# Kernel optimization log

Hardware: AMD Instinct MI355X
Metric: run time of the kernel (lower is better)

## Reference

```python
import jax, jax.numpy as jnp
import numpy as np

N_NODES = 50000
N_EDGES = 800000
IN_DIM = 128
HID_DIM = 128
N_GRAPHS = 512


def setup_inputs() -> dict:
    key = jax.random.key(0)
    ks = jax.random.split(key, 8)
    x = jax.random.normal(ks[0], (N_NODES, IN_DIM), dtype=jnp.float32)
    edge_index = jax.random.randint(ks[1], (2, N_EDGES), 0, N_NODES, dtype=jnp.int64)
    batch = jnp.sort(jax.random.randint(ks[2], (N_NODES,), 0, N_GRAPHS, dtype=jnp.int64))
    x_source = jax.random.randint(ks[3], (N_NODES,), 0, 2, dtype=jnp.int64)
    s1 = 1.0 / np.sqrt(IN_DIM)
    s2 = 1.0 / np.sqrt(HID_DIM)
    W1 = jax.random.normal(ks[4], (IN_DIM, HID_DIM), dtype=jnp.float32) * s1
    b1 = jnp.zeros((HID_DIM,), dtype=jnp.float32)
    W2 = jax.random.normal(ks[5], (HID_DIM, HID_DIM), dtype=jnp.float32) * s2
    b2 = jnp.zeros((HID_DIM,), dtype=jnp.float32)
    Wh = jax.random.normal(ks[6], (HID_DIM + IN_DIM, 2), dtype=jnp.float32) * (1.0 / np.sqrt(HID_DIM + IN_DIM))
    bh = jnp.zeros((2,), dtype=jnp.float32)
    return {"x": x, "edge_index": edge_index, "batch": batch, "x_source": x_source,
            "W1": W1, "b1": b1, "W2": W2, "b2": b2, "Wh": Wh, "bh": bh}


def _gcn_conv(x, W, b, src, dst, deg_inv_sqrt):
    # PyG GCNConv: h = x W; out[i] = sum_{j->i} norm_ij h[j] + norm_ii h[i] + b
    # with self-loops and symmetric normalization norm_ij = d_i^{-1/2} d_j^{-1/2}
    h = x @ W                                        # [N, out]
    norm_e = deg_inv_sqrt[src] * deg_inv_sqrt[dst]    # [E]
    msg = h[src] * norm_e[:, None]                    # gather + scale
    agg = jax.ops.segment_sum(msg, dst, num_segments=x.shape[0])
    agg = agg + h * (deg_inv_sqrt ** 2)[:, None]      # self-loop term
    return agg + b


def _mean_pool(x, seg, num_segments):
    sums = jax.ops.segment_sum(x, seg, num_segments=num_segments)
    cnt = jax.ops.segment_sum(jnp.ones((x.shape[0],), x.dtype), seg, num_segments=num_segments)
    return sums / jnp.maximum(cnt, 1.0)[:, None]


def reference(x, edge_index, batch, x_source, W1, b1, W2, b2, Wh, bh):
    src, dst = edge_index[0], edge_index[1]
    # degree with self-loops (edge weights = 1)
    deg = jax.ops.segment_sum(jnp.ones((src.shape[0],), x.dtype), dst,
                              num_segments=x.shape[0]) + 1.0
    deg_inv_sqrt = jax.lax.rsqrt(deg)

    h = jax.nn.relu(_gcn_conv(x, W1, b1, src, dst, deg_inv_sqrt))
    # dropout is identity in eval mode
    h = jax.nn.relu(_gcn_conv(h, W2, b2, src, dst, deg_inv_sqrt))

    gnn_emb = _mean_pool(h, batch, N_GRAPHS)          # [G, hid]

    # CodeBERT pooling: masked mean of raw node features where x_source == 1
    mask = (x_source == 1).astype(x.dtype)            # [N]
    summed = jax.ops.segment_sum(x * mask[:, None], batch, num_segments=N_GRAPHS)
    counts = jnp.maximum(jax.ops.segment_sum(mask, batch, num_segments=N_GRAPHS), 1.0)
    codebert_emb = summed / counts[:, None]           # [G, in]

    emb = jnp.concatenate([gnn_emb, codebert_emb], axis=1)  # [G, hid+in]
    return emb @ Wh + bh                              # [G, 2]
```

## Files before the change

### kernel.cpp

```cpp
#include <hip/hip_runtime.h>
#include <hip/hip_fp16.h>

#define NNODES 50000
#define NEDGES 800000
#define DIM    128
#define NGRAPH 512
#define NB_SCAN 196
#define NSLAB  3125

typedef _Float16 f16x8 __attribute__((ext_vector_type(8)));
typedef float    f32x4 __attribute__((ext_vector_type(4)));
union U4H8 { uint4 u; f16x8 h; };

__global__ void prep(int4* __restrict__ degp4,
                     const float* __restrict__ W1, const float* __restrict__ W2,
                     __half* __restrict__ Wt1, __half* __restrict__ Wt2) {
    int t = blockIdx.x * 256 + threadIdx.x;
    if (t < NNODES * 4) { degp4[t] = make_int4(0, 0, 0, 0); return; }
    int i = t - NNODES * 4;
    if (i >= 4096) return;
    const float* W = (i < 2048) ? W1 : W2;
    __half* Wt = (i < 2048) ? Wt1 : Wt2;
    int j = i & 2047;
    int c  = j >> 4;
    int k0 = (j & 15) * 8;
    __half tmp[8];
    #pragma unroll
    for (int u = 0; u < 8; ++u) tmp[u] = (__half)W[(size_t)(k0 + u) * DIM + c];
    *(uint4*)(Wt + (size_t)c * DIM + k0) = *(uint4*)tmp;
}

__global__ void edge_pos(const int4* __restrict__ dst4, int* __restrict__ degp,
                         int4* __restrict__ pos4, int n4) {
    int t = blockIdx.x * blockDim.x + threadIdx.x;
    if (t >= n4) return;
    int4 d = dst4[t];
    int4 p;
    p.x = atomicAdd(&degp[d.x << 4], 1);
    p.y = atomicAdd(&degp[d.y << 4], 1);
    p.z = atomicAdd(&degp[d.z << 4], 1);
    p.w = atomicAdd(&degp[d.w << 4], 1);
    pos4[t] = p;
}

__global__ void scan_block(const int* __restrict__ degp, int* __restrict__ out,
                           int* __restrict__ partials, float* __restrict__ dis, int n) {
    __shared__ int s[256];
    int t = threadIdx.x;
    int gid = blockIdx.x * 256 + t;
    int v = (gid < n) ? degp[gid << 4] : 0;
    if (gid < n) dis[gid] = rsqrtf((float)v + 1.0f);
    s[t] = v;
    __syncthreads();
    #pragma unroll
    for (int off = 1; off < 256; off <<= 1) {
        int u = (t >= off) ? s[t - off] : 0;
        __syncthreads();
        s[t] += u;
        __syncthreads();
    }
    if (gid < n) out[gid] = s[t] - v;
    if (t == 255) partials[blockIdx.x] = s[255];
}

__global__ void scan_partials(const int* __restrict__ in, int* __restrict__ out, int n) {
    __shared__ int s[256];
    int t = threadIdx.x;
    int v = (t < n) ? in[t] : 0;
    s[t] = v;
    __syncthreads();
    #pragma unroll
    for (int off = 1; off < 256; off <<= 1) {
        int u = (t >= off) ? s[t - off] : 0;
        __syncthreads();
        s[t] += u;
        __syncthreads();
    }
    if (t < n) out[t] = s[t] - v;
}

__global__ void edge_scatter2(const int4* __restrict__ src4, const int4* __restrict__ dst4,
                              const int4* __restrict__ pos4, const int* __restrict__ rowstart,
                              const int* __restrict__ part2, int* __restrict__ csr_src, int n4) {
    int t = blockIdx.x * blockDim.x + threadIdx.x;
    if (t >= n4) return;
    int4 s = src4[t];
    int4 d = dst4[t];
    int4 p = pos4[t];
    csr_src[rowstart[d.x] + part2[d.x >> 8] + p.x] = s.x;
    csr_src[rowstart[d.y] + part2[d.y >> 8] + p.y] = s.y;
    csr_src[rowstart[d.z] + part2[d.z >> 8] + p.z] = s.z;
    csr_src[rowstart[d.w] + part2[d.w >> 8] + p.w] = s.w;
}

template<typename XT>
__global__ void __launch_bounds__(256) gemm_mfma(const XT* __restrict__ X,
                                                 const __half* __restrict__ Wt,
                                                 const float* __restrict__ dis,
                                                 __half* __restrict__ Y) {
    __shared__ __align__(16) unsigned char Wl[128 * 256];

    const int t = threadIdx.x;
    {
        int col = t >> 1;
        int kb0 = (t & 1) * 128;
        const unsigned char* g = (const unsigned char*)Wt + col * 256 + kb0;
        #pragma unroll
        for (int i = 0; i < 8; ++i) {
            uint4 v = *(const uint4*)(g + i * 16);
            int kb = kb0 + i * 16;
            *(uint4*)(Wl + col * 256 + (kb ^ ((col & 7) << 4))) = v;
        }
    }
    __syncthreads();

    int wave = t >> 6;
    int slab = blockIdx.x * 4 + wave;
    if (slab >= NSLAB) return;
    int l  = t & 63;
    int lr = l & 15;
    int lg = l >> 4;

    int arow = slab * 16 + lr;

    f16x8 afr[4];
    if constexpr (sizeof(XT) == 4) {
        const float* xr = (const float*)X + (size_t)arow * DIM;
        #pragma unroll
        for (int c = 0; c < 4; ++c) {
            int k0 = c * 32 + lg * 8;
            float4 u0 = *(const float4*)(xr + k0);
            float4 u1 = *(const float4*)(xr + k0 + 4);
            f16x8 a;
            a[0] = (_Float16)u0.x; a[1] = (_Float16)u0.y;
            a[2] = (_Float16)u0.z; a[3] = (_Float16)u0.w;
            a[4] = (_Float16)u1.x; a[5] = (_Float16)u1.y;
            a[6] = (_Float16)u1.z; a[7] = (_Float16)u1.w;
            afr[c] = a;
        }
    } else {
        const __half* xr = (const __half*)X + (size_t)arow * DIM;
        #pragma unroll
        for (int c = 0; c < 4; ++c) {
            U4H8 u; u.u = *(const uint4*)(xr + c * 32 + lg * 8);
            afr[c] = u.h;
        }
    }

    f32x4 acc[8];
    #pragma unroll
    for (int jt = 0; jt < 8; ++jt) acc[jt] = (f32x4){0.f, 0.f, 0.f, 0.f};

    #pragma unroll
    for (int c = 0; c < 4; ++c) {
        #pragma unroll
        for (int jt = 0; jt < 8; ++jt) {
            int col = jt * 16 + lr;
            int kb  = c * 64 + lg * 16;
            U4H8 b;
            b.u = *(const uint4*)(Wl + col * 256 + (kb ^ ((col & 7) << 4)));
            acc[jt] = __builtin_amdgcn_mfma_f32_16x16x32_f16(afr[c], b.h, acc[jt], 0, 0, 0);
        }
    }

    float4 dv = *(const float4*)(dis + slab * 16 + lg * 4);
    float dsc[4] = {dv.x, dv.y, dv.z, dv.w};
    #pragma unroll
    for (int j = 0; j < 4; ++j) {
        int row = slab * 16 + lg * 4 + j;
        __half* yr = Y + (size_t)row * DIM + lr;
        #pragma unroll
        for (int jt = 0; jt < 8; ++jt)
            yr[jt * 16] = (__half)(acc[jt][j] * dsc[j]);
    }
}

__device__ __forceinline__ void acc_add(float4& a, uint2 u) {
    float2 f0 = __half22float2(*(__half2*)&u.x);
    float2 f1 = __half22float2(*(__half2*)&u.y);
    a.x += f0.x; a.y += f0.y; a.z += f1.x; a.w += f1.y;
}

__global__ void __launch_bounds__(256) gcn_gather(const __half* __restrict__ hwh,
                                                  const int* __restrict__ rowstart,
                                                  const int* __restrict__ part2,
                                                  const int* __restrict__ csr_src,
                                                  const float* __restrict__ dis,
                                                  const float* __restrict__ b,
                                                  __half* __restrict__ outh) {
    int t = blockIdx.x * 256 + threadIdx.x;
    int d = t >> 5, q = t & 31;
    if (d >= NNODES) return;
    const uint2* hw8 = (const uint2*)hwh;

    float4 a0 = make_float4(0.f, 0.f, 0.f, 0.f);
    float4 a1 = a0, a2 = a0, a3 = a0, a4 = a0, a5 = a0, a6 = a0, a7 = a0;

    acc_add(a0, hw8[(size_t)d * 32 + q]);

    int beg = rowstart[d] + part2[d >> 8];
    int end = (d + 1 < NNODES) ? rowstart[d + 1] + part2[(d + 1) >> 8] : NEDGES;
    int i = beg;
    for (; i + 8 <= end; i += 8) {
        int s0 = csr_src[i + 0], s1 = csr_src[i + 1];
        int s2 = csr_src[i + 2], s3 = csr_src[i + 3];
        int s4 = csr_src[i + 4], s5 = csr_src[i + 5];
        int s6 = csr_src[i + 6], s7 = csr_src[i + 7];
        uint2 v0 = hw8[(size_t)s0 * 32 + q];
        uint2 v1 = hw8[(size_t)s1 * 32 + q];
        uint2 v2 = hw8[(size_t)s2 * 32 + q];
        uint2 v3 = hw8[(size_t)s3 * 32 + q];
        uint2 v4 = hw8[(size_t)s4 * 32 + q];
        uint2 v5 = hw8[(size_t)s5 * 32 + q];
        uint2 v6 = hw8[(size_t)s6 * 32 + q];
        uint2 v7 = hw8[(size_t)s7 * 32 + q];
        acc_add(a0, v0); acc_add(a1, v1); acc_add(a2, v2); acc_add(a3, v3);
        acc_add(a4, v4); acc_add(a5, v5); acc_add(a6, v6); acc_add(a7, v7);
    }
    for (; i + 2 <= end; i += 2) {
        uint2 v0 = hw8[(size_t)csr_src[i + 0] * 32 + q];
        uint2 v1 = hw8[(size_t)csr_src[i + 1] * 32 + q];
        acc_add(a0, v0); acc_add(a1, v1);
    }
    if (i < end) acc_add(a0, hw8[(size_t)csr_src[i] * 32 + q]);

    a0.x += a1.x + a2.x + a3.x + a4.x + a5.x + a6.x + a7.x;
    a0.y += a1.y + a2.y + a3.y + a4.y + a5.y + a6.y + a7.y;
    a0.z += a1.z + a2.z + a3.z + a4.z + a5.z + a6.z + a7.z;
    a0.w += a1.w + a2.w + a3.w + a4.w + a5.w + a6.w + a7.w;

    float dd = dis[d];
    float4 bb = ((const float4*)b)[q];
    __half ot[4];
    ot[0] = (__half)fmaxf(fmaf(a0.x, dd, bb.x), 0.f);
    ot[1] = (__half)fmaxf(fmaf(a0.y, dd, bb.y), 0.f);
    ot[2] = (__half)fmaxf(fmaf(a0.z, dd, bb.z), 0.f);
    ot[3] = (__half)fmaxf(fmaf(a0.w, dd, bb.w), 0.f);
    ((uint2*)outh)[(size_t)d * 32 + q] = *(uint2*)ot;
}

__device__ __forceinline__ int lower_bound_i(const int* __restrict__ a, int n, int v) {
    int lo = 0, hi = n;
    while (lo < hi) {
        int mid = (lo + hi) >> 1;
        if (a[mid] < v) lo = mid + 1; else hi = mid;
    }
    return lo;
}

__global__ void __launch_bounds__(256) pool_head(const __half* __restrict__ h,
                                                 const float* __restrict__ x,
                                                 const int* __restrict__ batch,
                                                 const int* __restrict__ xsrc,
                                                 const float* __restrict__ Wh,
                                                 const float* __restrict__ bh,
                                                 float* __restrict__ out) {
    __shared__ float sAG[DIM];
    __shared__ float sAC[DIM];
    __shared__ int   sSC;
    int g   = blockIdx.x;
    int t   = threadIdx.x;
    int sub = t >> 5;
    int q   = t & 31;

    if (t < DIM) { sAG[t] = 0.f; sAC[t] = 0.f; }
    if (t == 0) sSC = 0;
    __syncthreads();

    int lo = lower_bound_i(batch, NNODES, g);
    int hi = lower_bound_i(batch, NNODES, g + 1);

    float4 ag = make_float4(0.f, 0.f, 0.f, 0.f);
    float4 ac = make_float4(0.f, 0.f, 0.f, 0.f);
    int sc = 0;
    const uint2* h8 = (const uint2*)h;
    const float4* x4 = (const float4*)x;
    for (int r = lo + sub; r < hi; r += 8) {
        acc_add(ag, h8[(size_t)r * 32 + q]);
        if (xsrc[r] == 1) {
            float4 xv = x4[(size_t)r * 32 + q];
            ac.x += xv.x; ac.y += xv.y; ac.z += xv.z; ac.w += xv.w;
            sc++;
        }
    }
    float* agp = sAG + q * 4;
    atomicAdd(agp + 0, ag.x); atomicAdd(agp + 1, ag.y);
    atomicAdd(agp + 2, ag.z); atomicAdd(agp + 3, ag.w);
    float* acp = sAC + q * 4;
    atomicAdd(acp + 0, ac.x); atomicAdd(acp + 1, ac.y);
    atomicAdd(acp + 2, ac.z); atomicAdd(acp + 3, ac.w);
    if (q == 0 && sc) atomicAdd(&sSC, sc);
    __syncthreads();

    if (t < 32) {
        float invg = 1.0f / fmaxf((float)(hi - lo), 1.0f);
        float invc = 1.0f / fmaxf((float)sSC, 1.0f);
        const float2* Wh2 = (const float2*)Wh;
        float a0 = 0.f, a1 = 0.f;
        #pragma unroll
        for (int j = 0; j < 4; ++j) {
            float e1 = sAG[t * 4 + j] * invg;
            float2 w1 = Wh2[t * 4 + j];
            a0 = fmaf(e1, w1.x, a0);
            a1 = fmaf(e1, w1.y, a1);
            float e2 = sAC[t * 4 + j] * invc;
            float2 w2 = Wh2[DIM + t * 4 + j];
            a0 = fmaf(e2, w2.x, a0);
            a1 = fmaf(e2, w2.y, a1);
        }
        #pragma unroll
        for (int off = 16; off; off >>= 1) {
            a0 += __shfl_down(a0, off, 32);
            a1 += __shfl_down(a1, off, 32);
        }
        if (t == 0) {
            out[g * 2 + 0] = a0 + bh[0];
            out[g * 2 + 1] = a1 + bh[1];
        }
    }
}

extern "C" void kernel_launch(void* const* d_in, const int* in_sizes, int n_in,
                              void* d_out, int out_size, void* d_ws, size_t ws_size,
                              hipStream_t stream) {
    const float* x     = (const float*)d_in[0];
    const int*   ei    = (const int*)d_in[1];
    const int*   batch = (const int*)d_in[2];
    const int*   xsrc  = (const int*)d_in[3];
    const float* W1 = (const float*)d_in[4];
    const float* b1 = (const float*)d_in[5];
    const float* W2 = (const float*)d_in[6];
    const float* b2 = (const float*)d_in[7];
    const float* Wh = (const float*)d_in[8];
    const float* bh = (const float*)d_in[9];
    float* out = (float*)d_out;

    const int* src = ei;
    const int* dst = ei + NEDGES;

    float* ws = (float*)d_ws;
    size_t off = 0;
    float*  dis      = ws + off;            off += 50048;
    int*    rowstart = (int*)(ws + off);    off += 50048;
    int*    degp     = (int*)(ws + off);    off += NNODES * 16;
    int*    part1    = (int*)(ws + off);    off += 256;
    int*    part2    = (int*)(ws + off);    off += 256;
    int*    pos      = (int*)(ws + off);    off += 800000;
    int*    csr_src  = (int*)(ws + off);    off += 800000;
    __half* Wt1      = (__half*)(ws + off); off += 8192;
    __half* Wt2      = (__half*)(ws + off); off += 8192;
    __half* hwh      = (__half*)(ws + off); off += (size_t)NNODES * DIM / 2;
    __half* hbuf     = (__half*)(ws + off); off += (size_t)NNODES * DIM / 2;

    const int n4 = NEDGES / 4;

    prep<<<(NNODES * 4 + 4096 + 255) / 256, 256, 0, stream>>>((int4*)degp, W1, W2, Wt1, Wt2);
    edge_pos<<<(n4 + 255) / 256, 256, 0, stream>>>((const int4*)dst, degp, (int4*)pos, n4);
    scan_block<<<NB_SCAN, 256, 0, stream>>>(degp, rowstart, part1, dis, NNODES);
    scan_partials<<<1, 256, 0, stream>>>(part1, part2, NB_SCAN);
    edge_scatter2<<<(n4 + 255) / 256, 256, 0, stream>>>((const int4*)src, (const int4*)dst,
                                                        (const int4*)pos, rowstart, part2,
                                                        csr_src, n4);

    const int ngemm = (NSLAB + 3) / 4;

    gemm_mfma<float><<<ngemm, 256, 0, stream>>>(x, Wt1, dis, hwh);
    gcn_gather<<<(NNODES * 32) / 256, 256, 0, stream>>>(hwh, rowstart, part2, csr_src, dis, b1, hbuf);

    gemm_mfma<__half><<<ngemm, 256, 0, stream>>>(hbuf, Wt2, dis, hwh);
    gcn_gather<<<(NNODES * 32) / 256, 256, 0, stream>>>(hwh, rowstart, part2, csr_src, dis, b2, hbuf);

    pool_head<<<NGRAPH, 256, 0, stream>>>(hbuf, x, batch, xsrc, Wh, bh, out);
}
```

Before: 173.6 us.

## Privatize degree counters into eight per-block-group copies to cut atomic contention

Result: slower. 177.9 us (+2.5%).

```diff
diff --git a/kernel.cpp b/kernel.cpp
--- a/kernel.cpp
+++ b/kernel.cpp
@@ -7,17 +7,20 @@
 #define NGRAPH 512
 #define NB_SCAN 196
 #define NSLAB  3125
+#define NPART  8
+#define CSTRIDE 50048
 
 typedef _Float16 f16x8 __attribute__((ext_vector_type(8)));
 typedef float    f32x4 __attribute__((ext_vector_type(4)));
 union U4H8 { uint4 u; f16x8 h; };
 
-__global__ void prep(int4* __restrict__ degp4,
+__global__ void prep(int4* __restrict__ cnt4,
                      const float* __restrict__ W1, const float* __restrict__ W2,
                      __half* __restrict__ Wt1, __half* __restrict__ Wt2) {
     int t = blockIdx.x * 256 + threadIdx.x;
-    if (t < NNODES * 4) { degp4[t] = make_int4(0, 0, 0, 0); return; }
-    int i = t - NNODES * 4;
+    const int nzero = NPART * CSTRIDE / 4;
+    if (t < nzero) { cnt4[t] = make_int4(0, 0, 0, 0); return; }
+    int i = t - nzero;
     if (i >= 4096) return;
     const float* W = (i < 2048) ? W1 : W2;
     __half* Wt = (i < 2048) ? Wt1 : Wt2;
@@ -30,26 +33,40 @@
     *(uint4*)(Wt + (size_t)c * DIM + k0) = *(uint4*)tmp;
 }
 
-__global__ void edge_pos(const int4* __restrict__ dst4, int* __restrict__ degp,
+__global__ void edge_pos(const int4* __restrict__ dst4, int* __restrict__ cnt8,
                          int4* __restrict__ pos4, int n4) {
     int t = blockIdx.x * blockDim.x + threadIdx.x;
     if (t >= n4) return;
+    int* c = cnt8 + (blockIdx.x & (NPART - 1)) * CSTRIDE;
     int4 d = dst4[t];
     int4 p;
-    p.x = atomicAdd(&degp[d.x << 4], 1);
-    p.y = atomicAdd(&degp[d.y << 4], 1);
-    p.z = atomicAdd(&degp[d.z << 4], 1);
-    p.w = atomicAdd(&degp[d.w << 4], 1);
+    p.x = atomicAdd(&c[d.x], 1);
+    p.y = atomicAdd(&c[d.y], 1);
+    p.z = atomicAdd(&c[d.z], 1);
+    p.w = atomicAdd(&c[d.w], 1);
     pos4[t] = p;
 }
 
-__global__ void scan_block(const int* __restrict__ degp, int* __restrict__ out,
-                           int* __restrict__ partials, float* __restrict__ dis, int n) {
+__global__ void scan_block(const int* __restrict__ cnt8, int* __restrict__ out,
+                           int* __restrict__ partials, float* __restrict__ dis,
+                           int* __restrict__ pre8, int n) {
     __shared__ int s[256];
     int t = threadIdx.x;
     int gid = blockIdx.x * 256 + t;
-    int v = (gid < n) ? degp[gid << 4] : 0;
-    if (gid < n) dis[gid] = rsqrtf((float)v + 1.0f);
+    int v = 0;
+    if (gid < n) {
+        int c[NPART];
+        #pragma unroll
+        for (int p = 0; p < NPART; ++p) c[p] = cnt8[p * CSTRIDE + gid];
+        int pr[NPART];
+        int run = 0;
+        #pragma unroll
+        for (int p = 0; p < NPART; ++p) { pr[p] = run; run += c[p]; }
+        v = run;
+        *(int4*)(pre8 + (size_t)gid * 8)     = make_int4(pr[0], pr[1], pr[2], pr[3]);
+        *(int4*)(pre8 + (size_t)gid * 8 + 4) = make_int4(pr[4], pr[5], pr[6], pr[7]);
+        dis[gid] = rsqrtf((float)v + 1.0f);
+    }
     s[t] = v;
     __syncthreads();
     #pragma unroll
@@ -81,16 +98,18 @@
 
 __global__ void edge_scatter2(const int4* __restrict__ src4, const int4* __restrict__ dst4,
                               const int4* __restrict__ pos4, const int* __restrict__ rowstart,
-                              const int* __restrict__ part2, int* __restrict__ csr_src, int n4) {
+                              const int* __restrict__ part2, const int* __restrict__ pre8,
+                              int* __restrict__ csr_src, int n4) {
     int t = blockIdx.x * blockDim.x + threadIdx.x;
     if (t >= n4) return;
+    int p = blockIdx.x & (NPART - 1);
     int4 s = src4[t];
     int4 d = dst4[t];
-    int4 p = pos4[t];
-    csr_src[rowstart[d.x] + part2[d.x >> 8] + p.x] = s.x;
-    csr_src[rowstart[d.y] + part2[d.y >> 8] + p.y] = s.y;
-    csr_src[rowstart[d.z] + part2[d.z >> 8] + p.z] = s.z;
-    csr_src[rowstart[d.w] + part2[d.w >> 8] + p.w] = s.w;
+    int4 q = pos4[t];
+    csr_src[rowstart[d.x] + part2[d.x >> 8] + pre8[(size_t)d.x * 8 + p] + q.x] = s.x;
+    csr_src[rowstart[d.y] + part2[d.y >> 8] + pre8[(size_t)d.y * 8 + p] + q.y] = s.y;
+    csr_src[rowstart[d.z] + part2[d.z >> 8] + pre8[(size_t)d.z * 8 + p] + q.z] = s.z;
+    csr_src[rowstart[d.w] + part2[d.w >> 8] + pre8[(size_t)d.w * 8 + p] + q.w] = s.w;
 }
 
 template<typename XT>
@@ -342,7 +361,8 @@
     size_t off = 0;
     float*  dis      = ws + off;            off += 50048;
     int*    rowstart = (int*)(ws + off);    off += 50048;
-    int*    degp     = (int*)(ws + off);    off += NNODES * 16;
+    int*    cnt8     = (int*)(ws + off);    off += NPART * CSTRIDE;
+    int*    pre8     = (int*)(ws + off);    off += 400384;
     int*    part1    = (int*)(ws + off);    off += 256;
     int*    part2    = (int*)(ws + off);    off += 256;
     int*    pos      = (int*)(ws + off);    off += 800000;
@@ -354,12 +374,12 @@
 
     const int n4 = NEDGES / 4;
 
-    prep<<<(NNODES * 4 + 4096 + 255) / 256, 256, 0, stream>>>((int4*)degp, W1, W2, Wt1, Wt2);
-    edge_pos<<<(n4 + 255) / 256, 256, 0, stream>>>((const int4*)dst, degp, (int4*)pos, n4);
-    scan_block<<<NB_SCAN, 256, 0, stream>>>(degp, rowstart, part1, dis, NNODES);
+    prep<<<(NPART * CSTRIDE / 4 + 4096 + 255) / 256, 256, 0, stream>>>((int4*)cnt8, W1, W2, Wt1, Wt2);
+    edge_pos<<<(n4 + 255) / 256, 256, 0, stream>>>((const int4*)dst, cnt8, (int4*)pos, n4);
+    scan_block<<<NB_SCAN, 256, 0, stream>>>(cnt8, rowstart, part1, dis, pre8, NNODES);
     scan_partials<<<1, 256, 0, stream>>>(part1, part2, NB_SCAN);
     edge_scatter2<<<(n4 + 255) / 256, 256, 0, stream>>>((const int4*)src, (const int4*)dst,
-                                                        (const int4*)pos, rowstart, part2,
+                                                        (const int4*)pos, rowstart, part2, pre8,
                                                         csr_src, n4);
 
     const int ngemm = (NSLAB + 3) / 4;
```

## Build CSR via two-level bucket sort instead of global atomic counting

Applied to the files above, without the earlier changes.

After: 151.1 us. 13.0% less time.

```diff
diff --git a/kernel.cpp b/kernel.cpp
--- a/kernel.cpp
+++ b/kernel.cpp
@@ -5,19 +5,21 @@
 #define NEDGES 800000
 #define DIM    128
 #define NGRAPH 512
-#define NB_SCAN 196
 #define NSLAB  3125
+#define EPB    1024
+#define NBLK_E 782
+#define NBUCK  196
+#define HSTRIDE NBLK_E
+#define NHIST  (NBUCK * HSTRIDE)
+#define NSB1   ((NHIST + 255) / 256)
 
 typedef _Float16 f16x8 __attribute__((ext_vector_type(8)));
 typedef float    f32x4 __attribute__((ext_vector_type(4)));
 union U4H8 { uint4 u; f16x8 h; };
 
-__global__ void prep(int4* __restrict__ degp4,
-                     const float* __restrict__ W1, const float* __restrict__ W2,
-                     __half* __restrict__ Wt1, __half* __restrict__ Wt2) {
-    int t = blockIdx.x * 256 + threadIdx.x;
-    if (t < NNODES * 4) { degp4[t] = make_int4(0, 0, 0, 0); return; }
-    int i = t - NNODES * 4;
+__global__ void prep_w(const float* __restrict__ W1, const float* __restrict__ W2,
+                       __half* __restrict__ Wt1, __half* __restrict__ Wt2) {
+    int i = blockIdx.x * 256 + threadIdx.x;
     if (i >= 4096) return;
     const float* W = (i < 2048) ? W1 : W2;
     __half* Wt = (i < 2048) ? Wt1 : Wt2;
@@ -30,67 +32,123 @@
     *(uint4*)(Wt + (size_t)c * DIM + k0) = *(uint4*)tmp;
 }
 
-__global__ void edge_pos(const int4* __restrict__ dst4, int* __restrict__ degp,
-                         int4* __restrict__ pos4, int n4) {
-    int t = blockIdx.x * blockDim.x + threadIdx.x;
-    if (t >= n4) return;
-    int4 d = dst4[t];
-    int4 p;
-    p.x = atomicAdd(&degp[d.x << 4], 1);
-    p.y = atomicAdd(&degp[d.y << 4], 1);
-    p.z = atomicAdd(&degp[d.z << 4], 1);
-    p.w = atomicAdd(&degp[d.w << 4], 1);
-    pos4[t] = p;
-}
-
-__global__ void scan_block(const int* __restrict__ degp, int* __restrict__ out,
-                           int* __restrict__ partials, float* __restrict__ dis, int n) {
+__global__ void __launch_bounds__(256) bucket_hist(const int* __restrict__ dst,
+                                                   int* __restrict__ hist) {
+    __shared__ int cnt[NBUCK];
+    int t = threadIdx.x;
+    if (t < NBUCK) cnt[t] = 0;
+    __syncthreads();
+    int e0 = blockIdx.x * EPB + t * 4;
+    if (e0 + 3 < NEDGES) {
+        int4 d = *(const int4*)(dst + e0);
+        atomicAdd(&cnt[d.x >> 8], 1);
+        atomicAdd(&cnt[d.y >> 8], 1);
+        atomicAdd(&cnt[d.z >> 8], 1);
+        atomicAdd(&cnt[d.w >> 8], 1);
+    }
+    __syncthreads();
+    if (t < NBUCK) hist[t * HSTRIDE + blockIdx.x] = cnt[t];
+}
+
+__global__ void sb1(const int* __restrict__ in, int* __restrict__ out,
+                    int* __restrict__ partials) {
     __shared__ int s[256];
     int t = threadIdx.x;
     int gid = blockIdx.x * 256 + t;
-    int v = (gid < n) ? degp[gid << 4] : 0;
-    if (gid < n) dis[gid] = rsqrtf((float)v + 1.0f);
+    int v = (gid < NHIST) ? in[gid] : 0;
     s[t] = v;
     __syncthreads();
     #pragma unroll
-    for (int off = 1; off < 256; off <<= 1) {
-        int u = (t >= off) ? s[t - off] : 0;
+    for (int o = 1; o < 256; o <<= 1) {
+        int u = (t >= o) ? s[t - o] : 0;
         __syncthreads();
         s[t] += u;
         __syncthreads();
     }
-    if (gid < n) out[gid] = s[t] - v;
+    if (gid < NHIST) out[gid] = s[t] - v;
     if (t == 255) partials[blockIdx.x] = s[255];
 }
 
-__global__ void scan_partials(const int* __restrict__ in, int* __restrict__ out, int n) {
-    __shared__ int s[256];
+__global__ void sb2(int* __restrict__ partials) {
+    __shared__ int s[1024];
     int t = threadIdx.x;
-    int v = (t < n) ? in[t] : 0;
+    int v = (t < NSB1) ? partials[t] : 0;
     s[t] = v;
     __syncthreads();
     #pragma unroll
-    for (int off = 1; off < 256; off <<= 1) {
-        int u = (t >= off) ? s[t - off] : 0;
+    for (int o = 1; o < 1024; o <<= 1) {
+        int u = (t >= o) ? s[t - o] : 0;
         __syncthreads();
         s[t] += u;
         __syncthreads();
     }
-    if (t < n) out[t] = s[t] - v;
-}
-
-__global__ void edge_scatter2(const int4* __restrict__ src4, const int4* __restrict__ dst4,
-                              const int4* __restrict__ pos4, const int* __restrict__ rowstart,
-                              const int* __restrict__ part2, int* __restrict__ csr_src, int n4) {
-    int t = blockIdx.x * blockDim.x + threadIdx.x;
-    if (t >= n4) return;
-    int4 s = src4[t];
-    int4 d = dst4[t];
-    int4 p = pos4[t];
-    csr_src[rowstart[d.x] + part2[d.x >> 8] + p.x] = s.x;
-    csr_src[rowstart[d.y] + part2[d.y >> 8] + p.y] = s.y;
-    csr_src[rowstart[d.z] + part2[d.z >> 8] + p.z] = s.z;
-    csr_src[rowstart[d.w] + part2[d.w >> 8] + p.w] = s.w;
+    if (t < NSB1) partials[t] = s[t] - v;
+}
+
+__global__ void sb3(int* __restrict__ hist, const int* __restrict__ partials) {
+    int gid = blockIdx.x * 256 + threadIdx.x;
+    if (gid < NHIST) hist[gid] += partials[blockIdx.x];
+}
+
+__global__ void __launch_bounds__(256) bucket_scatter(const int* __restrict__ src,
+                                                      const int* __restrict__ dst,
+                                                      const int* __restrict__ hist,
+                                                      int2* __restrict__ ebuf) {
+    __shared__ int cnt[NBUCK];
+    __shared__ int base[NBUCK];
+    int t = threadIdx.x;
+    if (t < NBUCK) { cnt[t] = 0; base[t] = hist[t * HSTRIDE + blockIdx.x]; }
+    __syncthreads();
+    int e0 = blockIdx.x * EPB + t * 4;
+    if (e0 + 3 < NEDGES) {
+        int4 s = *(const int4*)(src + e0);
+        int4 d = *(const int4*)(dst + e0);
+        int b, r;
+        b = d.x >> 8; r = atomicAdd(&cnt[b], 1); ebuf[base[b] + r] = make_int2(s.x, d.x);
+        b = d.y >> 8; r = atomicAdd(&cnt[b], 1); ebuf[base[b] + r] = make_int2(s.y, d.y);
+        b = d.z >> 8; r = atomicAdd(&cnt[b], 1); ebuf[base[b] + r] = make_int2(s.z, d.z);
+        b = d.w >> 8; r = atomicAdd(&cnt[b], 1); ebuf[base[b] + r] = make_int2(s.w, d.w);
+    }
+}
+
+__global__ void __launch_bounds__(256) node_sort(const int2* __restrict__ ebuf,
+                                                 const int* __restrict__ hist,
+                                                 int* __restrict__ rowstart,
+                                                 float* __restrict__ dis,
+                                                 int* __restrict__ csr_src) {
+    __shared__ int cnt[256], cnt2[256], off[256], s[256];
+    int b = blockIdx.x;
+    int t = threadIdx.x;
+    int start = hist[b * HSTRIDE];
+    int end = (b + 1 < NBUCK) ? hist[(b + 1) * HSTRIDE] : NEDGES;
+    cnt[t] = 0; cnt2[t] = 0;
+    __syncthreads();
+    for (int i = start + t; i < end; i += 256)
+        atomicAdd(&cnt[ebuf[i].y & 255], 1);
+    __syncthreads();
+    s[t] = cnt[t];
+    __syncthreads();
+    #pragma unroll
+    for (int o = 1; o < 256; o <<= 1) {
+        int u = (t >= o) ? s[t - o] : 0;
+        __syncthreads();
+        s[t] += u;
+        __syncthreads();
+    }
+    off[t] = s[t] - cnt[t];
+    int node = b * 256 + t;
+    if (node < NNODES) {
+        rowstart[node] = start + off[t];
+        dis[node] = rsqrtf((float)cnt[t] + 1.0f);
+    }
+    if (b == NBUCK - 1 && t == 0) rowstart[NNODES] = NEDGES;
+    __syncthreads();
+    for (int i = start + t; i < end; i += 256) {
+        int2 e = ebuf[i];
+        int j = e.y & 255;
+        int r = atomicAdd(&cnt2[j], 1);
+        csr_src[start + off[j] + r] = e.x;
+    }
 }
 
 template<typename XT>
@@ -157,9 +215,9 @@
         for (int jt = 0; jt < 8; ++jt) {
             int col = jt * 16 + lr;
             int kb  = c * 64 + lg * 16;
-            U4H8 b;
-            b.u = *(const uint4*)(Wl + col * 256 + (kb ^ ((col & 7) << 4)));
-            acc[jt] = __builtin_amdgcn_mfma_f32_16x16x32_f16(afr[c], b.h, acc[jt], 0, 0, 0);
+            U4H8 bb;
+            bb.u = *(const uint4*)(Wl + col * 256 + (kb ^ ((col & 7) << 4)));
+            acc[jt] = __builtin_amdgcn_mfma_f32_16x16x32_f16(afr[c], bb.h, acc[jt], 0, 0, 0);
         }
     }
 
@@ -183,7 +241,6 @@
 
 __global__ void __launch_bounds__(256) gcn_gather(const __half* __restrict__ hwh,
                                                   const int* __restrict__ rowstart,
-                                                  const int* __restrict__ part2,
                                                   const int* __restrict__ csr_src,
                                                   const float* __restrict__ dis,
                                                   const float* __restrict__ b,
@@ -198,8 +255,7 @@
 
     acc_add(a0, hw8[(size_t)d * 32 + q]);
 
-    int beg = rowstart[d] + part2[d >> 8];
-    int end = (d + 1 < NNODES) ? rowstart[d + 1] + part2[(d + 1) >> 8] : NEDGES;
+    int beg = rowstart[d], end = rowstart[d + 1];
     int i = beg;
     for (; i + 8 <= end; i += 8) {
         int s0 = csr_src[i + 0], s1 = csr_src[i + 1];
@@ -342,33 +398,30 @@
     size_t off = 0;
     float*  dis      = ws + off;            off += 50048;
     int*    rowstart = (int*)(ws + off);    off += 50048;
-    int*    degp     = (int*)(ws + off);    off += NNODES * 16;
-    int*    part1    = (int*)(ws + off);    off += 256;
-    int*    part2    = (int*)(ws + off);    off += 256;
-    int*    pos      = (int*)(ws + off);    off += 800000;
+    int*    hist     = (int*)(ws + off);    off += ((NHIST + 255) & ~255);
+    int*    partials = (int*)(ws + off);    off += 1024;
+    int2*   ebuf     = (int2*)(ws + off);   off += 2 * 800000;
     int*    csr_src  = (int*)(ws + off);    off += 800000;
     __half* Wt1      = (__half*)(ws + off); off += 8192;
     __half* Wt2      = (__half*)(ws + off); off += 8192;
     __half* hwh      = (__half*)(ws + off); off += (size_t)NNODES * DIM / 2;
     __half* hbuf     = (__half*)(ws + off); off += (size_t)NNODES * DIM / 2;
 
-    const int n4 = NEDGES / 4;
-
-    prep<<<(NNODES * 4 + 4096 + 255) / 256, 256, 0, stream>>>((int4*)degp, W1, W2, Wt1, Wt2);
-    edge_pos<<<(n4 + 255) / 256, 256, 0, stream>>>((const int4*)dst, degp, (int4*)pos, n4);
-    scan_block<<<NB_SCAN, 256, 0, stream>>>(degp, rowstart, part1, dis, NNODES);
-    scan_partials<<<1, 256, 0, stream>>>(part1, part2, NB_SCAN);
-    edge_scatter2<<<(n4 + 255) / 256, 256, 0, stream>>>((const int4*)src, (const int4*)dst,
-                                                        (const int4*)pos, rowstart, part2,
-                                                        csr_src, n4);
+    prep_w<<<16, 256, 0, stream>>>(W1, W2, Wt1, Wt2);
+    bucket_hist<<<NBLK_E, 256, 0, stream>>>(dst, hist);
+    sb1<<<NSB1, 256, 0, stream>>>(hist, hist, partials);
+    sb2<<<1, 1024, 0, stream>>>(partials);
+    sb3<<<NSB1, 256, 0, stream>>>(hist, partials);
+    bucket_scatter<<<NBLK_E, 256, 0, stream>>>(src, dst, hist, ebuf);
+    node_sort<<<NBUCK, 256, 0, stream>>>(ebuf, hist, rowstart, dis, csr_src);
 
     const int ngemm = (NSLAB + 3) / 4;
 
     gemm_mfma<float><<<ngemm, 256, 0, stream>>>(x, Wt1, dis, hwh);
-    gcn_gather<<<(NNODES * 32) / 256, 256, 0, stream>>>(hwh, rowstart, part2, csr_src, dis, b1, hbuf);
+    gcn_gather<<<(NNODES * 32) / 256, 256, 0, stream>>>(hwh, rowstart, csr_src, dis, b1, hbuf);
 
     gemm_mfma<__half><<<ngemm, 256, 0, stream>>>(hbuf, Wt2, dis, hwh);
-    gcn_gather<<<(NNODES * 32) / 256, 256, 0, stream>>>(hwh, rowstart, part2, csr_src, dis, b2, hbuf);
+    gcn_gather<<<(NNODES * 32) / 256, 256, 0, stream>>>(hwh, rowstart, csr_src, dis, b2, hbuf);
 
     pool_head<<<NGRAPH, 256, 0, stream>>>(hbuf, x, batch, xsrc, Wh, bh, out);
 }
```
